# Kernel tuning notes

Measured on AMD Instinct MI355X. Metric: run time of the kernel, lower is better.

## Reference

```python
import jax, jax.numpy as jnp
import numpy as np

NUM_BINS_X = 1024
NUM_BINS_Y = 1024
XL, XH, YL, YH = 0.0, 1024.0, 0.0, 1024.0
NUM_NODES = 4_000_000
NUM_FILLER = 1_000_000
NUM_PHYS = NUM_NODES - NUM_FILLER      # physical = movable + fixed
NUM_MOVABLE = 2_500_000
UNIT_PIN_CAPACITY = 2.0                # pins per unit area capacity
PIN_STRETCH_RATIO = 1.414              # DREAMPlace default sqrt(2)
MAX_ADJ = 2.5
MIN_ADJ = 1.0 / MAX_ADJ
SPAN = 4                               # max bins any box spans per axis (sizes <= 2*bin)


def setup_inputs() -> dict:
    key = jax.random.key(0)
    k1, k2, k3, k4, k5 = jax.random.split(key, 5)
    node_size_x = 0.5 + 1.5 * jax.random.uniform(k1, (NUM_NODES,), jnp.float32)
    node_size_y = 0.5 + 1.5 * jax.random.uniform(k2, (NUM_NODES,), jnp.float32)
    pos_x = XL + jax.random.uniform(k3, (NUM_NODES,), jnp.float32) * (XH - XL - 2.0)
    pos_y = YL + jax.random.uniform(k4, (NUM_NODES,), jnp.float32) * (YH - YL - 2.0)
    pos = jnp.concatenate([pos_x, pos_y])  # [2*num_nodes], x then y
    pin_weights = jax.random.randint(k5, (NUM_PHYS,), 1, 9, jnp.int32)
    return {"pos": pos, "node_size_x": node_size_x, "node_size_y": node_size_y,
            "pin_weights": pin_weights}


def _overlap(lo, hi, bin_lo, bin_size):
    # overlap length of interval [lo,hi] with bin [bin_lo, bin_lo+bin_size]
    return jnp.clip(jnp.minimum(hi, bin_lo + bin_size) - jnp.maximum(lo, bin_lo), 0.0, None)


def reference(pos, node_size_x, node_size_y, pin_weights):
    bsx = (XH - XL) / NUM_BINS_X
    bsy = (YH - YL) / NUM_BINS_Y
    dtype = pos.dtype

    # ---- phase 1: pin density map over stretched boxes of physical nodes ----
    sx = node_size_x[:NUM_PHYS]
    sy = node_size_y[:NUM_PHYS]
    hx = 0.5 * jnp.maximum(bsx * PIN_STRETCH_RATIO, sx)  # half stretched extent
    hy = 0.5 * jnp.maximum(bsy * PIN_STRETCH_RATIO, sy)
    cx = pos[:NUM_PHYS] + 0.5 * sx
    cy = pos[NUM_NODES:NUM_NODES + NUM_PHYS] + 0.5 * sy
    xmin, xmax = cx - hx, cx + hx
    ymin, ymax = cy - hy, cy + hy
    dens = pin_weights.astype(dtype) / (4.0 * hx * hy)   # pins per unit area

    bxl = jnp.clip(jnp.floor((xmin - XL) / bsx).astype(jnp.int32), 0, NUM_BINS_X - 1)
    byl = jnp.clip(jnp.floor((ymin - YL) / bsy).astype(jnp.int32), 0, NUM_BINS_Y - 1)

    pmap = jnp.zeros(NUM_BINS_X * NUM_BINS_Y, dtype)
    for di in range(SPAN):
        bx = bxl + di
        ox = _overlap(xmin, xmax, XL + bx.astype(dtype) * bsx, bsx)
        vx = bx < NUM_BINS_X
        for dj in range(SPAN):
            by = byl + dj
            oy = _overlap(ymin, ymax, YL + by.astype(dtype) * bsy, bsy)
            v = vx & (by < NUM_BINS_Y)
            idx = jnp.where(v, bx * NUM_BINS_Y + by, 0)
            val = jnp.where(v, dens * ox * oy, 0.0)
            pmap = pmap.at[idx].add(val)

    # density -> utilization: scatter added pins*overlap/area, divide by bin area
    pmap = pmap / (bsx * bsy)
    adj = jnp.clip(pmap / UNIT_PIN_CAPACITY, MIN_ADJ, MAX_ADJ)

    # ---- phase 2: per-movable-node pin-optimized area over actual footprint ----
    mx = pos[:NUM_MOVABLE]
    my = pos[NUM_NODES:NUM_NODES + NUM_MOVABLE]
    msx = node_size_x[:NUM_MOVABLE]
    msy = node_size_y[:NUM_MOVABLE]
    bxl2 = jnp.clip(jnp.floor((mx - XL) / bsx).astype(jnp.int32), 0, NUM_BINS_X - 1)
    byl2 = jnp.clip(jnp.floor((my - YL) / bsy).astype(jnp.int32), 0, NUM_BINS_Y - 1)

    area = jnp.zeros(NUM_MOVABLE, dtype)
    for di in range(SPAN):
        bx = bxl2 + di
        ox = _overlap(mx, mx + msx, XL + bx.astype(dtype) * bsx, bsx)
        vx = bx < NUM_BINS_X
        for dj in range(SPAN):
            by = byl2 + dj
            oy = _overlap(my, my + msy, YL + by.astype(dtype) * bsy, bsy)
            v = vx & (by < NUM_BINS_Y)
            idx = jnp.where(v, bx * NUM_BINS_Y + by, 0)
            area = area + jnp.where(v, ox * oy * adj[idx], 0.0)
    return area
```

## Files before the change

### kernel.cpp

```cpp
#include <hip/hip_runtime.h>

#define NBX 1024
#define NBY 1024
#define TS 64
#define NTX (NBX / TS)
#define NTY (NBY / TS)
#define NTILES (NTX * NTY)
#define LW 66
#define LSTRIDE 67
#define CAP 13056
#define CAPM 11008

#define FB_BLOCK 512
#define FB_K 8
#define FB_CHUNK (FB_BLOCK * FB_K)

#define SPLIT 2

#define PMAP_SCALE 131072.0f
#define PMAP_INV   (1.0f / 131072.0f)

static constexpr int NUM_NODES   = 4000000;
static constexpr int NUM_PHYS    = 3000000;
static constexpr int NUM_MOVABLE = 2500000;
static constexpr int HALF_MOV    = NUM_MOVABLE / 2;

typedef unsigned long long u64;

static constexpr size_t OFF_PMAP  = 0;
static constexpr size_t OFF_CURS  = OFF_PMAP + (size_t)NBX * NBY * 4;
static constexpr size_t OFF_CURSM = OFF_CURS + NTILES * 4;
static constexpr size_t OFF_SLAB  = ((OFF_CURSM + NTILES * 4 + 15) / 16) * 16;
static constexpr size_t OFF_MSLAB = ((OFF_SLAB + (size_t)NTILES * CAP * 8 + 15) / 16) * 16;
static constexpr size_t WS_FULL   = OFF_MSLAB + (size_t)NTILES * CAPM * 12;

__global__ void __launch_bounds__(FB_BLOCK)
fill_both(const float* __restrict__ pos, const float* __restrict__ nsx,
          const float* __restrict__ nsy, const int* __restrict__ pw,
          unsigned* __restrict__ curs, unsigned* __restrict__ cursm,
          uint2* __restrict__ slab, uint3* __restrict__ mslab,
          float* __restrict__ pmap) {
    __shared__ unsigned cntp[NTILES], cntm[NTILES];
    __shared__ unsigned offp[NTILES], offm[NTILES];
    __shared__ unsigned Dp[NTILES], Dm[NTILES];
    __shared__ unsigned wsum[8];
    __shared__ uint2 SAB[FB_CHUNK];
    __shared__ unsigned char  STb[FB_CHUNK];
    __shared__ unsigned short SO[FB_CHUNK];

    const int tid = threadIdx.x;
    const int b0  = blockIdx.x * FB_CHUNK;

    {
        const int NP4 = (NBX * NBY) / 4;
        int per = (NP4 + gridDim.x - 1) / gridDim.x;
        int s = blockIdx.x * per;
        int e = min(s + per, NP4);
        float4* p4 = (float4*)pmap;
        for (int c = s + tid; c < e; c += FB_BLOCK)
            p4[c] = make_float4(0.f, 0.f, 0.f, 0.f);
    }

    if (tid < NTILES) { cntp[tid] = 0u; cntm[tid] = 0u; }
    __syncthreads();

    u64 P[FB_K];
    u64 M[FB_K];
    int TPM[FB_K];
    unsigned rkP[FB_K], rkM[FB_K];

    #pragma unroll
    for (int k = 0; k < FB_K; ++k) {
        int i = b0 + k * FB_BLOCK + tid;
        int tp = -1, tm = -1;
        if (i < NUM_PHYS) {
            float mx = pos[i], my = pos[NUM_NODES + i];
            float sx = nsx[i], sy = nsy[i];
            float hx = 0.5f * fmaxf(1.414f, sx);
            float hy = 0.5f * fmaxf(1.414f, sy);
            unsigned qhx = (unsigned)__float2int_rn((hx - 0.7f) * 1024.0f);
            unsigned qhy = (unsigned)__float2int_rn((hy - 0.7f) * 1024.0f);
            float hxd = 0.7f + (float)qhx * (1.0f / 1024.0f);
            float hyd = 0.7f + (float)qhy * (1.0f / 1024.0f);
            float xmin = mx + 0.5f * sx - hxd;
            float ymin = my + 0.5f * sy - hyd;
            int bxl = min(max((int)floorf(xmin), 0), NBX - 1);
            int byl = min(max((int)floorf(ymin), 0), NBY - 1);
            tp = (bxl >> 6) * NTY + (byl >> 6);
            int bx0 = (tp >> 4) << 6, by0 = (tp & 15) << 6;
            unsigned ex = (unsigned)__float2int_rn((xmin - (float)bx0 + 1.0f) * 8192.0f);
            unsigned ey = (unsigned)__float2int_rn((ymin - (float)by0 + 1.0f) * 8192.0f);
            P[k] = (u64)ex | ((u64)ey << 20) | ((u64)qhx << 40)
                 | ((u64)qhy << 50) | ((u64)(unsigned)(pw[i] - 1) << 60);
            rkP[k] = atomicAdd(&cntp[tp], 1u);
            if (i < NUM_MOVABLE) {
                int bxm = min(max((int)floorf(mx), 0), NBX - 1);
                int bym = min(max((int)floorf(my), 0), NBY - 1);
                tm = (bxm >> 6) * NTY + (bym >> 6);
                int bx0m = (tm >> 4) << 6, by0m = (tm & 15) << 6;
                unsigned exm = (unsigned)__float2int_rn((mx - (float)bx0m) * 8192.0f);
                unsigned eym = (unsigned)__float2int_rn((my - (float)by0m) * 8192.0f);
                unsigned qsx = (unsigned)__float2int_rn((sx - 0.5f) * 2048.0f);
                unsigned qsy = (unsigned)__float2int_rn((sy - 0.5f) * 2048.0f);
                M[k] = (u64)exm | ((u64)eym << 20) | ((u64)qsx << 40) | ((u64)qsy << 52);
                rkM[k] = atomicAdd(&cntm[tm], 1u);
            }
        }
        TPM[k] = (tp & 0xffff) | (tm << 16);
    }
    __syncthreads();

    {
        const int lane   = tid & 63;
        const int scanId = tid & 255;
        const bool isMov = tid >= 256;

        unsigned v = isMov ? cntm[scanId] : cntp[scanId];
        unsigned x = v;
        #pragma unroll
        for (int d = 1; d < 64; d <<= 1) {
            unsigned y = __shfl_up(x, d);
            if (lane >= d) x += y;
        }
        if (lane == 63) wsum[tid >> 6] = x;
        __syncthreads();
        unsigned add = 0;
        const int w0 = isMov ? 4 : 0;
        for (int w = 0; w < (scanId >> 6); ++w) add += wsum[w0 + w];
        unsigned o = x + add - v;
        unsigned* gc = isMov ? cursm : curs;
        unsigned base = v ? atomicAdd(&gc[scanId], v) : 0u;
        if (isMov) { offm[scanId] = o; Dm[scanId] = base - o; }
        else       { offp[scanId] = o; Dp[scanId] = base - o; }
    }
    __syncthreads();

    #pragma unroll
    for (int k = 0; k < FB_K; ++k) {
        int tp = (int)(short)(TPM[k] & 0xffff);
        if (tp >= 0) {
            unsigned s = offp[tp] + rkP[k];
            SAB[s] = make_uint2((unsigned)P[k], (unsigned)(P[k] >> 32));
            STb[s] = (unsigned char)tp;
        }
    }
    __syncthreads();

    {
        unsigned tot = offp[NTILES - 1] + cntp[NTILES - 1];
        for (unsigned j = tid; j < tot; j += FB_BLOCK) {
            unsigned tile = STb[j];
            unsigned p = Dp[tile] + j;
            if (p < CAP)
                slab[(size_t)tile * CAP + p] = SAB[j];
        }
    }
    __syncthreads();

    #pragma unroll
    for (int k = 0; k < FB_K; ++k) {
        int tm = TPM[k] >> 16;
        if (tm >= 0) {
            unsigned s = offm[tm] + rkM[k];
            SAB[s] = make_uint2((unsigned)M[k], (unsigned)(M[k] >> 32));
            SO[s]  = (unsigned short)(k * FB_BLOCK + tid);
            STb[s] = (unsigned char)tm;
        }
    }
    __syncthreads();

    {
        unsigned tot = offm[NTILES - 1] + cntm[NTILES - 1];
        for (unsigned j = tid; j < tot; j += FB_BLOCK) {
            unsigned tile = STb[j];
            unsigned p = Dm[tile] + j;
            if (p < CAPM) {
                uint2 ab = SAB[j];
                mslab[(size_t)tile * CAPM + p] =
                    make_uint3(ab.x, ab.y, (unsigned)(b0 + SO[j]));
            }
        }
    }
}

__global__ void __launch_bounds__(1024)
tile_scatter(const uint2* __restrict__ slab, const unsigned* __restrict__ curs,
             float* __restrict__ pmap) {
    __shared__ unsigned lds[LW * LSTRIDE];
    int t   = blockIdx.x / SPLIT;
    int sub = blockIdx.x - t * SPLIT;
    int bx0 = (t >> 4) << 6, by0 = (t & 15) << 6;

    for (int c = threadIdx.x; c < LW * LSTRIDE; c += 1024) lds[c] = 0u;
    __syncthreads();

    unsigned n = min(curs[t], (unsigned)CAP);
    const uint2* sl = slab + (size_t)t * CAP;

    unsigned k = threadIdx.x + sub * 1024;
    uint2 p = (k < n) ? sl[k] : make_uint2(0u, 0u);
    while (k < n) {
        unsigned kn = k + SPLIT * 1024;
        uint2 pn = (kn < n) ? sl[kn] : make_uint2(0u, 0u);

        u64 P = (u64)p.x | ((u64)p.y << 32);
        float xminl = (float)(P & 0xFFFFFu)         * (1.0f / 8192.0f) - 1.0f;
        float yminl = (float)((P >> 20) & 0xFFFFFu) * (1.0f / 8192.0f) - 1.0f;
        float hx = 0.7f + (float)((P >> 40) & 0x3FFu) * (1.0f / 1024.0f);
        float hy = 0.7f + (float)((P >> 50) & 0x3FFu) * (1.0f / 1024.0f);
        float pwv  = (float)(1u + (unsigned)(P >> 60));
        float dens = pwv / (4.0f * hx * hy);
        float xmaxl = xminl + 2.0f * hx;
        float ymaxl = yminl + 2.0f * hy;

        int lx0 = min(max((int)floorf(xminl), 0), TS - 1);
        int ly0 = min(max((int)floorf(yminl), 0), TS - 1);
        #pragma unroll
        for (int di = 0; di < 3; ++di) {
            float bl = (float)(lx0 + di);
            float ox = fminf(xmaxl, bl + 1.0f) - fmaxf(xminl, bl);
            if (ox <= 0.0f) continue;
            float dox = dens * ox;
            #pragma unroll
            for (int dj = 0; dj < 3; ++dj) {
                float bly = (float)(ly0 + dj);
                float oy  = fminf(ymaxl, bly + 1.0f) - fmaxf(yminl, bly);
                if (oy > 0.0f) {
                    unsigned q = (unsigned)__float2int_rn(dox * oy * PMAP_SCALE);
                    atomicAdd(&lds[(lx0 + di) * LSTRIDE + (ly0 + dj)], q);
                }
            }
        }
        p = pn;
        k = kn;
    }
    __syncthreads();

    for (int c = threadIdx.x; c < LW * LW; c += 1024) {
        int lx = c / LW, ly = c - lx * LW;
        int bx = bx0 + lx, by = by0 + ly;
        if (bx >= NBX || by >= NBY) continue;
        float v = (float)lds[lx * LSTRIDE + ly] * PMAP_INV;
        if (v != 0.0f)
            atomicAdd(&pmap[bx * NBY + by], v);
    }
}

__global__ void __launch_bounds__(1024)
gather_tile(const uint3* __restrict__ mslab, const unsigned* __restrict__ cursm,
            const float* __restrict__ pmap, float* __restrict__ out) {
    __shared__ float adj[LW * LSTRIDE];
    int t   = blockIdx.x / SPLIT;
    int sub = blockIdx.x - t * SPLIT;
    int bx0 = (t >> 4) << 6, by0 = (t & 15) << 6;

    for (int c = threadIdx.x; c < LW * LW; c += 1024) {
        int r = c / LW, col = c - r * LW;
        int bx = min(bx0 + r,  NBX - 1);
        int by = min(by0 + col, NBY - 1);
        adj[r * LSTRIDE + col] =
            fminf(fmaxf(pmap[bx * NBY + by] * 0.5f, 0.4f), 2.5f);
    }
    __syncthreads();

    unsigned n = min(cursm[t], (unsigned)CAPM);
    const uint3* sl = mslab + (size_t)t * CAPM;

    for (unsigned k = threadIdx.x + sub * 1024; k < n; k += SPLIT * 1024) {
        uint3 p = sl[k];
        u64 M = (u64)p.x | ((u64)p.y << 32);
        float mxl = (float)(M & 0xFFFFFu)         * (1.0f / 8192.0f);
        float myl = (float)((M >> 20) & 0xFFFFFu) * (1.0f / 8192.0f);
        float sx  = 0.5f + (float)((M >> 40) & 0xFFFu) * (1.0f / 2048.0f);
        float sy  = 0.5f + (float)(M >> 52)            * (1.0f / 2048.0f);
        float xmaxl = mxl + sx;
        float ymaxl = myl + sy;

        int lx0 = min((int)mxl, TS - 1);
        int ly0 = min((int)myl, TS - 1);

        float area = 0.0f;
        #pragma unroll
        for (int di = 0; di < 3; ++di) {
            float bl = (float)(lx0 + di);
            float ox = fmaxf(fminf(xmaxl, bl + 1.0f) - fmaxf(mxl, bl), 0.0f);
            #pragma unroll
            for (int dj = 0; dj < 3; ++dj) {
                float bly = (float)(ly0 + dj);
                float oy  = fmaxf(fminf(ymaxl, bly + 1.0f) - fmaxf(myl, bly), 0.0f);
                area += ox * oy * adj[(lx0 + di) * LSTRIDE + (ly0 + dj)];
            }
        }
        out[p.z] = area;
    }
}

__global__ void __launch_bounds__(256)
scatter_pin(const float* __restrict__ pos, const float* __restrict__ nsx,
            const float* __restrict__ nsy, const int* __restrict__ pw,
            float* __restrict__ pmap) {
    int i = blockIdx.x * blockDim.x + threadIdx.x;
    if (i >= NUM_PHYS) return;
    float sx = nsx[i], sy = nsy[i];
    float hx = 0.5f * fmaxf(1.414f, sx);
    float hy = 0.5f * fmaxf(1.414f, sy);
    float cx = pos[i] + 0.5f * sx;
    float cy = pos[NUM_NODES + i] + 0.5f * sy;
    float xmin = cx - hx, xmax = cx + hx;
    float ymin = cy - hy, ymax = cy + hy;
    float dens = (float)pw[i] / (4.0f * hx * hy);
    int bxl = min(max((int)floorf(xmin), 0), NBX - 1);
    int byl = min(max((int)floorf(ymin), 0), NBY - 1);
    #pragma unroll
    for (int di = 0; di < 3; ++di) {
        float bl = (float)(bxl + di);
        float ox = fminf(xmax, bl + 1.0f) - fmaxf(xmin, bl);
        if (ox <= 0.0f) continue;
        float dox = dens * ox;
        int base = min(bxl + di, NBX - 1) * NBY;
        #pragma unroll
        for (int dj = 0; dj < 3; ++dj) {
            float bly = (float)(byl + dj);
            float oy  = fminf(ymax, bly + 1.0f) - fmaxf(ymin, bly);
            if (oy > 0.0f) atomicAdd(&pmap[base + min(byl + dj, NBY - 1)], dox * oy);
        }
    }
}

__device__ __forceinline__ float gather_one(const float* __restrict__ pos,
                                            const float* __restrict__ nsx,
                                            const float* __restrict__ nsy,
                                            const float* __restrict__ pmap,
                                            int i) {
    float mx = pos[i];
    float my = pos[NUM_NODES + i];
    float xmax = mx + nsx[i];
    float ymax = my + nsy[i];
    int bxl = min(max((int)floorf(mx), 0), NBX - 1);
    int byl = min(max((int)floorf(my), 0), NBY - 1);
    float ox[3], oy[3];
    int rowb[3], colb[3];
    #pragma unroll
    for (int d = 0; d < 3; ++d) {
        float bl  = (float)(bxl + d);
        float bly = (float)(byl + d);
        ox[d] = fmaxf(fminf(xmax, bl + 1.0f) - fmaxf(mx, bl), 0.0f);
        oy[d] = fmaxf(fminf(ymax, bly + 1.0f) - fmaxf(my, bly), 0.0f);
        rowb[d] = min(bxl + d, NBX - 1) * NBY;
        colb[d] = min(byl + d, NBY - 1);
    }
    float area = 0.0f;
    #pragma unroll
    for (int di = 0; di < 3; ++di)
        #pragma unroll
        for (int dj = 0; dj < 3; ++dj) {
            float a = fminf(fmaxf(pmap[rowb[di] + colb[dj]] * 0.5f, 0.4f), 2.5f);
            area += ox[di] * oy[dj] * a;
        }
    return area;
}

__global__ void __launch_bounds__(256)
gather_area(const float* __restrict__ pos, const float* __restrict__ nsx,
            const float* __restrict__ nsy, const float* __restrict__ pmap,
            float* __restrict__ out) {
    int i = blockIdx.x * blockDim.x + threadIdx.x;
    if (i >= HALF_MOV) return;
    int i2 = i + HALF_MOV;
    float a1 = gather_one(pos, nsx, nsy, pmap, i);
    float a2 = gather_one(pos, nsx, nsy, pmap, i2);
    out[i]  = a1;
    out[i2] = a2;
}

extern "C" void kernel_launch(void* const* d_in, const int* in_sizes, int n_in,
                              void* d_out, int out_size, void* d_ws, size_t ws_size,
                              hipStream_t stream) {
    const float* pos = (const float*)d_in[0];
    const float* nsx = (const float*)d_in[1];
    const float* nsy = (const float*)d_in[2];
    const int*   pw  = (const int*)d_in[3];
    float* out = (float*)d_out;

    char* ws = (char*)d_ws;
    float*    pmap  = (float*)(ws + OFF_PMAP);
    unsigned* curs  = (unsigned*)(ws + OFF_CURS);
    unsigned* cursm = (unsigned*)(ws + OFF_CURSM);
    uint2*    slab  = (uint2*)(ws + OFF_SLAB);
    uint3*    mslab = (uint3*)(ws + OFF_MSLAB);

    if (ws_size >= WS_FULL) {
        hipMemsetAsync(ws + OFF_CURS, 0, OFF_SLAB - OFF_CURS, stream);
        int grid = (NUM_PHYS + FB_CHUNK - 1) / FB_CHUNK;
        fill_both   <<<grid, FB_BLOCK, 0, stream>>>(pos, nsx, nsy, pw,
                                                    curs, cursm, slab, mslab, pmap);
        tile_scatter<<<NTILES * SPLIT, 1024, 0, stream>>>(slab, curs, pmap);
        gather_tile <<<NTILES * SPLIT, 1024, 0, stream>>>(mslab, cursm, pmap, out);
    } else {
        hipMemsetAsync(pmap, 0, (size_t)NBX * NBY * sizeof(float), stream);
        scatter_pin <<<(NUM_PHYS + 255) / 256, 256, 0, stream>>>(pos, nsx, nsy, pw, pmap);
        gather_area <<<(HALF_MOV + 255) / 256, 256, 0, stream>>>(pos, nsx, nsy, pmap, out);
    }
}
```

Baseline: 175.5 us.

## Fuse pin scatter and area gather per tile using halo slabs

```diff
diff --git a/kernel.cpp b/kernel.cpp
--- a/kernel.cpp
+++ b/kernel.cpp
@@ -10,12 +10,11 @@
 #define LSTRIDE 67
 #define CAP 13056
 #define CAPM 11008
+#define HCAP 2048
 
 #define FB_BLOCK 512
 #define FB_K 8
 #define FB_CHUNK (FB_BLOCK * FB_K)
-
-#define SPLIT 2
 
 #define PMAP_SCALE 131072.0f
 #define PMAP_INV   (1.0f / 131072.0f)
@@ -30,16 +29,19 @@
 static constexpr size_t OFF_PMAP  = 0;
 static constexpr size_t OFF_CURS  = OFF_PMAP + (size_t)NBX * NBY * 4;
 static constexpr size_t OFF_CURSM = OFF_CURS + NTILES * 4;
-static constexpr size_t OFF_SLAB  = ((OFF_CURSM + NTILES * 4 + 15) / 16) * 16;
+static constexpr size_t OFF_CURH  = OFF_CURSM + NTILES * 4;
+static constexpr size_t OFF_SLAB  = ((OFF_CURH + NTILES * 4 + 15) / 16) * 16;
 static constexpr size_t OFF_MSLAB = ((OFF_SLAB + (size_t)NTILES * CAP * 8 + 15) / 16) * 16;
-static constexpr size_t WS_FULL   = OFF_MSLAB + (size_t)NTILES * CAPM * 12;
+static constexpr size_t OFF_HSLAB = ((OFF_MSLAB + (size_t)NTILES * CAPM * 12 + 15) / 16) * 16;
+static constexpr size_t WS_FULL   = OFF_HSLAB + (size_t)NTILES * HCAP * 8;
 
 __global__ void __launch_bounds__(FB_BLOCK)
 fill_both(const float* __restrict__ pos, const float* __restrict__ nsx,
           const float* __restrict__ nsy, const int* __restrict__ pw,
           unsigned* __restrict__ curs, unsigned* __restrict__ cursm,
+          unsigned* __restrict__ curh,
           uint2* __restrict__ slab, uint3* __restrict__ mslab,
-          float* __restrict__ pmap) {
+          uint2* __restrict__ hslab) {
     __shared__ unsigned cntp[NTILES], cntm[NTILES];
     __shared__ unsigned offp[NTILES], offm[NTILES];
     __shared__ unsigned Dp[NTILES], Dm[NTILES];
@@ -51,16 +53,6 @@
     const int tid = threadIdx.x;
     const int b0  = blockIdx.x * FB_CHUNK;
 
-    {
-        const int NP4 = (NBX * NBY) / 4;
-        int per = (NP4 + gridDim.x - 1) / gridDim.x;
-        int s = blockIdx.x * per;
-        int e = min(s + per, NP4);
-        float4* p4 = (float4*)pmap;
-        for (int c = s + tid; c < e; c += FB_BLOCK)
-            p4[c] = make_float4(0.f, 0.f, 0.f, 0.f);
-    }
-
     if (tid < NTILES) { cntp[tid] = 0u; cntm[tid] = 0u; }
     __syncthreads();
 
@@ -76,6 +68,7 @@
         if (i < NUM_PHYS) {
             float mx = pos[i], my = pos[NUM_NODES + i];
             float sx = nsx[i], sy = nsy[i];
+            int  pwv = pw[i];
             float hx = 0.5f * fmaxf(1.414f, sx);
             float hy = 0.5f * fmaxf(1.414f, sy);
             unsigned qhx = (unsigned)__float2int_rn((hx - 0.7f) * 1024.0f);
@@ -91,8 +84,36 @@
             unsigned ex = (unsigned)__float2int_rn((xmin - (float)bx0 + 1.0f) * 8192.0f);
             unsigned ey = (unsigned)__float2int_rn((ymin - (float)by0 + 1.0f) * 8192.0f);
             P[k] = (u64)ex | ((u64)ey << 20) | ((u64)qhx << 40)
-                 | ((u64)qhy << 50) | ((u64)(unsigned)(pw[i] - 1) << 60);
+                 | ((u64)qhy << 50) | ((u64)(unsigned)(pwv - 1) << 60);
             rkP[k] = atomicAdd(&cntp[tp], 1u);
+
+            {
+                int lx = bxl & 63, ly = byl & 63;
+                int dx = (lx < 2) ? -1 : ((lx >= 62) ? 1 : 0);
+                int dy = (ly < 2) ? -1 : ((ly >= 62) ? 1 : 0);
+                if ((dx | dy) != 0) {
+                    int tx = bxl >> 6, ty = byl >> 6;
+                    auto emitH = [&](int ttx, int tty) {
+                        int tt = ttx * NTY + tty;
+                        unsigned exh = (unsigned)__float2int_rn(
+                            (xmin - (float)(ttx << 6) + 2.0f) * 8192.0f);
+                        unsigned eyh = (unsigned)__float2int_rn(
+                            (ymin - (float)(tty << 6) + 2.0f) * 8192.0f);
+                        u64 H = (u64)exh | ((u64)eyh << 20) | ((u64)qhx << 40)
+                              | ((u64)qhy << 50) | ((u64)(unsigned)(pwv - 1) << 60);
+                        unsigned slot = atomicAdd(&curh[tt], 1u);
+                        if (slot < HCAP)
+                            hslab[(size_t)tt * HCAP + slot] =
+                                make_uint2((unsigned)H, (unsigned)(H >> 32));
+                    };
+                    bool okx = dx && (unsigned)(tx + dx) < (unsigned)NTX;
+                    bool oky = dy && (unsigned)(ty + dy) < (unsigned)NTY;
+                    if (okx) emitH(tx + dx, ty);
+                    if (oky) emitH(tx, ty + dy);
+                    if (okx && oky) emitH(tx + dx, ty + dy);
+                }
+            }
+
             if (i < NUM_MOVABLE) {
                 int bxm = min(max((int)floorf(mx), 0), NBX - 1);
                 int bym = min(max((int)floorf(my), 0), NBY - 1);
@@ -184,114 +205,137 @@
 }
 
 __global__ void __launch_bounds__(1024)
-tile_scatter(const uint2* __restrict__ slab, const unsigned* __restrict__ curs,
-             float* __restrict__ pmap) {
+fused_bc(const uint2* __restrict__ slab, const unsigned* __restrict__ curs,
+         const uint2* __restrict__ hslab, const unsigned* __restrict__ curh,
+         const uint3* __restrict__ mslab, const unsigned* __restrict__ cursm,
+         float* __restrict__ out) {
     __shared__ unsigned lds[LW * LSTRIDE];
-    int t   = blockIdx.x / SPLIT;
-    int sub = blockIdx.x - t * SPLIT;
-    int bx0 = (t >> 4) << 6, by0 = (t & 15) << 6;
-
-    for (int c = threadIdx.x; c < LW * LSTRIDE; c += 1024) lds[c] = 0u;
-    __syncthreads();
-
-    unsigned n = min(curs[t], (unsigned)CAP);
-    const uint2* sl = slab + (size_t)t * CAP;
-
-    unsigned k = threadIdx.x + sub * 1024;
-    uint2 p = (k < n) ? sl[k] : make_uint2(0u, 0u);
-    while (k < n) {
-        unsigned kn = k + SPLIT * 1024;
-        uint2 pn = (kn < n) ? sl[kn] : make_uint2(0u, 0u);
-
-        u64 P = (u64)p.x | ((u64)p.y << 32);
-        float xminl = (float)(P & 0xFFFFFu)         * (1.0f / 8192.0f) - 1.0f;
-        float yminl = (float)((P >> 20) & 0xFFFFFu) * (1.0f / 8192.0f) - 1.0f;
-        float hx = 0.7f + (float)((P >> 40) & 0x3FFu) * (1.0f / 1024.0f);
-        float hy = 0.7f + (float)((P >> 50) & 0x3FFu) * (1.0f / 1024.0f);
-        float pwv  = (float)(1u + (unsigned)(P >> 60));
-        float dens = pwv / (4.0f * hx * hy);
-        float xmaxl = xminl + 2.0f * hx;
-        float ymaxl = yminl + 2.0f * hy;
-
-        int lx0 = min(max((int)floorf(xminl), 0), TS - 1);
-        int ly0 = min(max((int)floorf(yminl), 0), TS - 1);
-        #pragma unroll
-        for (int di = 0; di < 3; ++di) {
-            float bl = (float)(lx0 + di);
-            float ox = fminf(xmaxl, bl + 1.0f) - fmaxf(xminl, bl);
-            if (ox <= 0.0f) continue;
-            float dox = dens * ox;
+    const int t   = blockIdx.x;
+    const int tid = threadIdx.x;
+
+    for (int c = tid; c < LW * LSTRIDE; c += 1024) lds[c] = 0u;
+    __syncthreads();
+
+    {
+        unsigned n = min(curs[t], (unsigned)CAP);
+        const uint2* sl = slab + (size_t)t * CAP;
+        unsigned k = tid;
+        uint2 p = (k < n) ? sl[k] : make_uint2(0u, 0u);
+        while (k < n) {
+            unsigned kn = k + 1024;
+            uint2 pn = (kn < n) ? sl[kn] : make_uint2(0u, 0u);
+
+            u64 P = (u64)p.x | ((u64)p.y << 32);
+            float xminl = (float)(P & 0xFFFFFu)         * (1.0f / 8192.0f) - 1.0f;
+            float yminl = (float)((P >> 20) & 0xFFFFFu) * (1.0f / 8192.0f) - 1.0f;
+            float hx = 0.7f + (float)((P >> 40) & 0x3FFu) * (1.0f / 1024.0f);
+            float hy = 0.7f + (float)((P >> 50) & 0x3FFu) * (1.0f / 1024.0f);
+            float pwv  = (float)(1u + (unsigned)(P >> 60));
+            float dens = pwv / (4.0f * hx * hy);
+            float xmaxl = xminl + 2.0f * hx;
+            float ymaxl = yminl + 2.0f * hy;
+
+            int lx0 = min(max((int)floorf(xminl), 0), TS - 1);
+            int ly0 = min(max((int)floorf(yminl), 0), TS - 1);
             #pragma unroll
-            for (int dj = 0; dj < 3; ++dj) {
-                float bly = (float)(ly0 + dj);
-                float oy  = fminf(ymaxl, bly + 1.0f) - fmaxf(yminl, bly);
-                if (oy > 0.0f) {
-                    unsigned q = (unsigned)__float2int_rn(dox * oy * PMAP_SCALE);
-                    atomicAdd(&lds[(lx0 + di) * LSTRIDE + (ly0 + dj)], q);
+            for (int di = 0; di < 3; ++di) {
+                float bl = (float)(lx0 + di);
+                float ox = fminf(xmaxl, bl + 1.0f) - fmaxf(xminl, bl);
+                if (ox <= 0.0f) continue;
+                float dox = dens * ox;
+                #pragma unroll
+                for (int dj = 0; dj < 3; ++dj) {
+                    float bly = (float)(ly0 + dj);
+                    float oy  = fminf(ymaxl, bly + 1.0f) - fmaxf(yminl, bly);
+                    if (oy > 0.0f) {
+                        unsigned q = (unsigned)__float2int_rn(dox * oy * PMAP_SCALE);
+                        atomicAdd(&lds[(lx0 + di) * LSTRIDE + (ly0 + dj)], q);
+                    }
                 }
             }
-        }
-        p = pn;
-        k = kn;
-    }
-    __syncthreads();
-
-    for (int c = threadIdx.x; c < LW * LW; c += 1024) {
-        int lx = c / LW, ly = c - lx * LW;
-        int bx = bx0 + lx, by = by0 + ly;
-        if (bx >= NBX || by >= NBY) continue;
-        float v = (float)lds[lx * LSTRIDE + ly] * PMAP_INV;
-        if (v != 0.0f)
-            atomicAdd(&pmap[bx * NBY + by], v);
-    }
-}
-
-__global__ void __launch_bounds__(1024)
-gather_tile(const uint3* __restrict__ mslab, const unsigned* __restrict__ cursm,
-            const float* __restrict__ pmap, float* __restrict__ out) {
-    __shared__ float adj[LW * LSTRIDE];
-    int t   = blockIdx.x / SPLIT;
-    int sub = blockIdx.x - t * SPLIT;
-    int bx0 = (t >> 4) << 6, by0 = (t & 15) << 6;
-
-    for (int c = threadIdx.x; c < LW * LW; c += 1024) {
-        int r = c / LW, col = c - r * LW;
-        int bx = min(bx0 + r,  NBX - 1);
-        int by = min(by0 + col, NBY - 1);
-        adj[r * LSTRIDE + col] =
-            fminf(fmaxf(pmap[bx * NBY + by] * 0.5f, 0.4f), 2.5f);
-    }
-    __syncthreads();
-
-    unsigned n = min(cursm[t], (unsigned)CAPM);
-    const uint3* sl = mslab + (size_t)t * CAPM;
-
-    for (unsigned k = threadIdx.x + sub * 1024; k < n; k += SPLIT * 1024) {
-        uint3 p = sl[k];
-        u64 M = (u64)p.x | ((u64)p.y << 32);
-        float mxl = (float)(M & 0xFFFFFu)         * (1.0f / 8192.0f);
-        float myl = (float)((M >> 20) & 0xFFFFFu) * (1.0f / 8192.0f);
-        float sx  = 0.5f + (float)((M >> 40) & 0xFFFu) * (1.0f / 2048.0f);
-        float sy  = 0.5f + (float)(M >> 52)            * (1.0f / 2048.0f);
-        float xmaxl = mxl + sx;
-        float ymaxl = myl + sy;
-
-        int lx0 = min((int)mxl, TS - 1);
-        int ly0 = min((int)myl, TS - 1);
-
-        float area = 0.0f;
-        #pragma unroll
-        for (int di = 0; di < 3; ++di) {
-            float bl = (float)(lx0 + di);
-            float ox = fmaxf(fminf(xmaxl, bl + 1.0f) - fmaxf(mxl, bl), 0.0f);
+            p = pn;
+            k = kn;
+        }
+    }
+
+    {
+        unsigned n = min(curh[t], (unsigned)HCAP);
+        const uint2* hl = hslab + (size_t)t * HCAP;
+        for (unsigned k = tid; k < n; k += 1024) {
+            uint2 p = hl[k];
+            u64 P = (u64)p.x | ((u64)p.y << 32);
+            float xminl = (float)(P & 0xFFFFFu)         * (1.0f / 8192.0f) - 2.0f;
+            float yminl = (float)((P >> 20) & 0xFFFFFu) * (1.0f / 8192.0f) - 2.0f;
+            float hx = 0.7f + (float)((P >> 40) & 0x3FFu) * (1.0f / 1024.0f);
+            float hy = 0.7f + (float)((P >> 50) & 0x3FFu) * (1.0f / 1024.0f);
+            float pwv  = (float)(1u + (unsigned)(P >> 60));
+            float dens = pwv / (4.0f * hx * hy);
+            float xmaxl = xminl + 2.0f * hx;
+            float ymaxl = yminl + 2.0f * hy;
+
+            int lx0 = (int)floorf(xminl);
+            int ly0 = (int)floorf(yminl);
             #pragma unroll
-            for (int dj = 0; dj < 3; ++dj) {
-                float bly = (float)(ly0 + dj);
-                float oy  = fmaxf(fminf(ymaxl, bly + 1.0f) - fmaxf(myl, bly), 0.0f);
-                area += ox * oy * adj[(lx0 + di) * LSTRIDE + (ly0 + dj)];
-            }
-        }
-        out[p.z] = area;
+            for (int di = 0; di < 3; ++di) {
+                int r = lx0 + di;
+                if ((unsigned)r >= (unsigned)LW) continue;
+                float bl = (float)r;
+                float ox = fminf(xmaxl, bl + 1.0f) - fmaxf(xminl, bl);
+                if (ox <= 0.0f) continue;
+                float dox = dens * ox;
+                #pragma unroll
+                for (int dj = 0; dj < 3; ++dj) {
+                    int cc = ly0 + dj;
+                    if ((unsigned)cc >= (unsigned)LW) continue;
+                    float bly = (float)cc;
+                    float oy  = fminf(ymaxl, bly + 1.0f) - fmaxf(yminl, bly);
+                    if (oy > 0.0f) {
+                        unsigned q = (unsigned)__float2int_rn(dox * oy * PMAP_SCALE);
+                        atomicAdd(&lds[r * LSTRIDE + cc], q);
+                    }
+                }
+            }
+        }
+    }
+    __syncthreads();
+
+    float* adjf = (float*)lds;
+    for (int c = tid; c < LW * LSTRIDE; c += 1024) {
+        float v = (float)lds[c] * PMAP_INV;
+        adjf[c] = fminf(fmaxf(v * 0.5f, 0.4f), 2.5f);
+    }
+    __syncthreads();
+
+    {
+        unsigned n = min(cursm[t], (unsigned)CAPM);
+        const uint3* sl = mslab + (size_t)t * CAPM;
+        for (unsigned k = tid; k < n; k += 1024) {
+            uint3 p = sl[k];
+            u64 M = (u64)p.x | ((u64)p.y << 32);
+            float mxl = (float)(M & 0xFFFFFu)         * (1.0f / 8192.0f);
+            float myl = (float)((M >> 20) & 0xFFFFFu) * (1.0f / 8192.0f);
+            float sx  = 0.5f + (float)((M >> 40) & 0xFFFu) * (1.0f / 2048.0f);
+            float sy  = 0.5f + (float)(M >> 52)            * (1.0f / 2048.0f);
+            float xmaxl = mxl + sx;
+            float ymaxl = myl + sy;
+
+            int lx0 = min((int)mxl, TS - 1);
+            int ly0 = min((int)myl, TS - 1);
+
+            float area = 0.0f;
+            #pragma unroll
+            for (int di = 0; di < 3; ++di) {
+                float bl = (float)(lx0 + di);
+                float ox = fmaxf(fminf(xmaxl, bl + 1.0f) - fmaxf(mxl, bl), 0.0f);
+                #pragma unroll
+                for (int dj = 0; dj < 3; ++dj) {
+                    float bly = (float)(ly0 + dj);
+                    float oy  = fmaxf(fminf(ymaxl, bly + 1.0f) - fmaxf(myl, bly), 0.0f);
+                    area += ox * oy * adjf[(lx0 + di) * LSTRIDE + (ly0 + dj)];
+                }
+            }
+            out[p.z] = area;
+        }
     }
 }
 
@@ -386,16 +430,19 @@
     float*    pmap  = (float*)(ws + OFF_PMAP);
     unsigned* curs  = (unsigned*)(ws + OFF_CURS);
     unsigned* cursm = (unsigned*)(ws + OFF_CURSM);
+    unsigned* curh  = (unsigned*)(ws + OFF_CURH);
     uint2*    slab  = (uint2*)(ws + OFF_SLAB);
     uint3*    mslab = (uint3*)(ws + OFF_MSLAB);
+    uint2*    hslab = (uint2*)(ws + OFF_HSLAB);
 
     if (ws_size >= WS_FULL) {
         hipMemsetAsync(ws + OFF_CURS, 0, OFF_SLAB - OFF_CURS, stream);
         int grid = (NUM_PHYS + FB_CHUNK - 1) / FB_CHUNK;
-        fill_both   <<<grid, FB_BLOCK, 0, stream>>>(pos, nsx, nsy, pw,
-                                                    curs, cursm, slab, mslab, pmap);
-        tile_scatter<<<NTILES * SPLIT, 1024, 0, stream>>>(slab, curs, pmap);
-        gather_tile <<<NTILES * SPLIT, 1024, 0, stream>>>(mslab, cursm, pmap, out);
+        fill_both<<<grid, FB_BLOCK, 0, stream>>>(pos, nsx, nsy, pw,
+                                                 curs, cursm, curh,
+                                                 slab, mslab, hslab);
+        fused_bc <<<NTILES, 1024, 0, stream>>>(slab, curs, hslab, curh,
+                                               mslab, cursm, out);
     } else {
         hipMemsetAsync(pmap, 0, (size_t)NBX * NBY * sizeof(float), stream);
         scatter_pin <<<(NUM_PHYS + 255) / 256, 256, 0, stream>>>(pos, nsx, nsy, pw, pmap);
```

Measured after the change: 544.5 us. 3.1x slower.
